# Performance work log

Hardware: AMD Instinct MI355X
Metric: run time of the kernel (lower is better)

## Reference

```python
import jax, jax.numpy as jnp
from jax import lax
import numpy as np

MAX_ATOMS = 50
MAX_DEGREE = 4
MAX_RINGS = 16
BATCH = 16384
EDGE_KEEP_PROB = 0.3  # fraction of neighbor slots that are real edges; rest are -1 (masked)


def setup_inputs() -> dict:
    key = jax.random.key(0)
    k1, k2 = jax.random.split(key)
    e = jax.random.randint(k1, (BATCH, MAX_ATOMS, MAX_DEGREE), 0, MAX_ATOMS, dtype=jnp.int32)
    keep = jax.random.uniform(k2, (BATCH, MAX_ATOMS, MAX_DEGREE)) < EDGE_KEEP_PROB
    edge = jnp.where(keep, e, jnp.int32(-1))
    return {"edge": edge}


def reference(edge):
    B, A, D = edge.shape
    N = A + 1  # node 0 is the masked-edge sentinel after +1 shift and zero-row pad
    bidx = jnp.arange(B)
    # masked_edges: shift indices by +1, pad a zero row at atom index 0 -> [B, N, D]
    me = jnp.pad(edge.astype(jnp.int32) + 1, ((0, 0), (1, 0), (0, 0)))

    # per-node state, shape [B, N]
    lnf = jnp.ones((B, N), jnp.int32).at[:, 0].set(0).at[:, 1].set(0)  # leaf_not_found
    nnv = jnp.ones((B, N), jnp.int32).at[:, 0].set(0)                  # node_not_visited
    Tree = jnp.zeros((B, N), jnp.int32)                                 # parent pointers
    num_rings = jnp.zeros((B,), jnp.int32)
    ring_idx = jnp.zeros((B, N, 2), jnp.int32)

    def visit(state, visiting):
        lnf, nnv, Tree, num_rings, ring_idx = state
        for d in range(D):  # small static degree loop (4)
            nxt = me[bidx, visiting, d]                 # [B]
            slnf = lnf[bidx, nxt]                       # specific_leaf_not_found
            slnv = nnv[bidx, nxt]                       # specific_leaf_not_visited
            cyc = (1 - slnf) * slnv * (nxt != 0).astype(jnp.int32)  # cycle_found
            ring_idx = ring_idx.at[bidx, num_rings, 0].add(visiting * cyc)
            ring_idx = ring_idx.at[bidx, num_rings, 1].add(nxt * cyc)
            num_rings = num_rings + cyc
            Tree = Tree.at[bidx, nxt].add(slnf * visiting)
            lnf = lnf.at[bidx, nxt].set(0)
        nnv = nnv.at[bidx, visiting].set(0)
        return (lnf, nnv, Tree, num_rings, ring_idx)

    # atom_idx == 1: visit node 1 (special-cased init above)
    state = visit((lnf, nnv, Tree, num_rings, ring_idx), jnp.ones((B,), jnp.int32))

    def atom_body(_, state):
        lnf, nnv = state[0], state[1]
        visiting = jnp.argmax(nnv * (1 - lnf), axis=-1).astype(jnp.int32)
        return visit(state, visiting)

    state = lax.fori_loop(2, A + 1, atom_body, state)
    lnf, nnv, Tree, num_rings, ring_idx = state

    max_num_rings = jnp.max(num_rings)
    rings = jnp.zeros((B, MAX_RINGS, A), jnp.int32)

    def ring_body(carry):
        i, rings = carry
        air = jnp.zeros((B,), jnp.int32)  # atom_in_ring_idx

        # branch 0: mark ancestor chain of ring endpoint 0
        start = ring_idx[:, i, 0]
        vb0 = jnp.zeros((B, N), jnp.int32).at[bidx, start].set(1)
        def mark0(_, c):
            vb0, start = c
            nxt = Tree[bidx, start]
            return (vb0.at[bidx, nxt].set(1), nxt)
        vb0, _ = lax.fori_loop(0, A, mark0, (vb0, start))

        # branch 1: walk ancestor chain of endpoint 1, emit atoms until chains meet
        start = ring_idx[:, i, 1]
        vb1 = jnp.zeros((B, N), jnp.int32).at[bidx, start].set(1)
        rings = rings.at[bidx, i, air].set(start)
        def b1(_, c):
            rings, vb1, start, air = c
            nxt = Tree[bidx, start]
            same = jnp.any(vb0 * vb1 == 1, axis=-1)
            nsv = (~same).astype(jnp.int32)
            air = air + nsv
            rings = rings.at[bidx, i, air].add(nxt * nsv)
            vb1 = vb1.at[bidx, nxt].set(1)
            return (rings, vb1, nxt, air)
        rings, vb1, _, air = lax.fori_loop(0, A, b1, (rings, vb1, start, air))

        # branch 2: walk endpoint-0 chain again, emit atoms until it meets branch 1
        start = ring_idx[:, i, 0]
        vb0b = jnp.zeros((B, N), jnp.int32).at[bidx, start].set(1)
        air = air + 1
        rings = rings.at[bidx, i, air].set(start)
        def b2(_, c):
            rings, vb0b, start, air = c
            nxt = Tree[bidx, start]
            vb0b = vb0b.at[bidx, nxt].set(1)
            same = jnp.any(vb0b * vb1 == 1, axis=-1)
            nsv = (~same).astype(jnp.int32)
            air = air + nsv
            rings = rings.at[bidx, i, air].add(nxt * nsv)
            return (rings, vb0b, nxt, air)
        rings, _, _, _ = lax.fori_loop(0, A, b2, (rings, vb0b, start, air))
        return (i + 1, rings)

    def ring_cond(carry):
        return carry[0] < max_num_rings

    _, rings = lax.while_loop(ring_cond, ring_body, (jnp.int32(0), rings))
    return (Tree, ring_idx, rings - 1)
```

## Files before the change

kernel.cpp:

```cpp
#include <hip/hip_runtime.h>
#include <stdint.h>

constexpr int BATCH = 16384;
constexpr int A     = 50;
constexpr int NN    = 51;
constexpr int MAXR  = 16;
constexpr int EPW   = 8;
constexpr int WPB   = 4;

__device__ __forceinline__ void prep_row(int lane, int dep,
    int s0lo, int s0hi, int s1lo, int s1hi, int pack, int i,
    int& pos, int& ta, int& tua, int& s0v)
{
    const uint64_t s0 = ((uint64_t)(uint32_t)__builtin_amdgcn_readlane(s0hi, i) << 32)
                      |  (uint32_t)__builtin_amdgcn_readlane(s0lo, i);
    const uint64_t s1 = ((uint64_t)(uint32_t)__builtin_amdgcn_readlane(s1hi, i) << 32)
                      |  (uint32_t)__builtin_amdgcn_readlane(s1lo, i);
    const int pk = __builtin_amdgcn_readlane(pack, i);
    const int dm = pk & 0xff, ds0 = (pk >> 8) & 0xff, ds1 = (pk >> 16) & 0xff;
    s0v = (pk >> 24) & 0xff;
    ta  = ds1 - dm;
    tua = ta + ds0 - dm;
    const bool on1 = ((s1 >> lane) & 1) && (dep >= dm);
    const bool on0 = ((s0 >> lane) & 1) && (dep >  dm);
    int p = on1 ? (ds1 - dep) : on0 ? (ta + 1 + ds0 - dep) : 63;
    pos = p < 63 ? p : 63;
}

__global__ __launch_bounds__(WPB * 64)
void fused_kernel(const int* __restrict__ edge, int* __restrict__ out)
{
    const int lane  = threadIdx.x & 63;
    const int wid   = threadIdx.x >> 6;
    const int gbase = (blockIdx.x * WPB + wid) * EPW;

    __shared__ uint32_t eds [WPB][EPW][NN];
    __shared__ uint16_t comb[WPB][EPW][128];

    {
        const uint4 z = make_uint4(0, 0, 0, 0);
        uint4* c16 = (uint4*)&comb[wid][0][0];
        c16[lane]      = z;
        c16[lane + 64] = z;
    }
    {
        const int4* e4 = (const int4*)edge + (size_t)gbase * A;
        #pragma unroll
        for (int k = 0; k < 7; ++k) {
            const int gi = k * 64 + lane;
            if (gi < EPW * A) {
                const int4 v = e4[gi];
                const int el = gi / A, n = gi - A * el;
                eds[wid][el][n] = (uint32_t)(v.x + 1) | ((uint32_t)(v.y + 1) << 8)
                                | ((uint32_t)(v.z + 1) << 16) | ((uint32_t)(v.w + 1) << 24);
            }
        }
    }

    const int  e  = lane >> 3;
    const int  d8 = lane & 7;
    const int  d  = d8 & 3;
    const bool hi = d8 >= 4;

    uint64_t L = (((uint64_t)1 << NN) - 1) & ~(uint64_t)3;
    uint64_t V = (((uint64_t)1 << NN) - 1) & ~(uint64_t)1;
    uint64_t M = 2;
    int visiting = 1, nr = 0;
    uint32_t w = eds[wid][e][0];

    #pragma unroll 1
    for (int it = 0; it < A; ++it) {
        const int n0 = w & 0xff, n1 = (w >> 8) & 0xff, n2 = (w >> 16) & 0xff, n3 = w >> 24;
        const uint64_t bu = ((uint64_t)1 << n0) | ((uint64_t)1 << n1)
                          | ((uint64_t)1 << n2) | ((uint64_t)1 << n3);
        const int myn = (w >> (8 * d)) & 0xff;
        const uint64_t bm = (uint64_t)1 << myn;
        const uint64_t visbit = (uint64_t)1 << visiting;
        const uint64_t Mn = (M | (V & bu)) & ~visbit;
        const bool dn = (Mn == 0);
        const uint64_t Msafe = dn ? (uint64_t)2 : Mn;
        const int nv = (int)__builtin_ctzll(Msafe);
        const uint32_t wn = eds[wid][e][nv - 1];
        const bool dup = ((d > 0) & (myn == n0)) | ((d > 1) & (myn == n1)) | ((d > 2) & (myn == n2));
        const bool fa  = ((L & bm) == 0) | dup;
        const bool cf  = fa & ((V & bm) != 0) & (myn != 0);
        const bool cb  = cf & !hi;
        const uint64_t Bc = __ballot(cb);
        const uint32_t qb = (uint32_t)(Bc >> (lane & 56)) & 0xfu;
        const int slot = nr + __builtin_popcount(qb & ((1u << d) - 1));
        nr += __builtin_popcount(qb);
        const bool p  = hi ? (cf & (slot < NN)) : !fa;
        const int idx = hi ? (64 + slot) : myn;
        if (p) comb[wid][e][idx] = (uint16_t)(visiting | (hi ? (myn << 8) : 0));
        L &= ~bu;
        V &= ~visbit;
        M = Mn; visiting = nv;
        w = dn ? 0u : wn;
        if (__ballot(!dn) == 0) break;
    }

    int*  otree = out;
    int2* oridx = (int2*)(out + (size_t)BATCH * NN);

    uint64_t MkE[EPW];
    int gE[EPW], r01E[EPW];
    #pragma unroll
    for (int e2 = 0; e2 < EPW; ++e2) {
        const int b = gbase + e2;
        const int f = (lane < NN) ? (int)comb[wid][e2][lane] : 0;
        const uint32_t pv = (lane < NN) ? (uint32_t)comb[wid][e2][64 + lane] : 0;
        MkE[e2] = ((uint64_t)1 << lane) | ((uint64_t)1 << f);
        gE[e2]  = f;
        r01E[e2] = (int)pv;
        if (lane < NN) {
            otree[(size_t)b * NN + lane] = f;
            oridx[(size_t)b * NN + lane] = make_int2((int)(pv & 0xff), (int)(pv >> 8));
        }
    }
    #pragma unroll
    for (int j6 = 0; j6 < 6; ++j6) {
        int lo8[EPW], hi8[EPW], gg8[EPW];
        #pragma unroll
        for (int e2 = 0; e2 < EPW; ++e2) {
            const int ad = gE[e2] << 2;
            lo8[e2] = __builtin_amdgcn_ds_bpermute(ad, (int)(uint32_t)MkE[e2]);
            hi8[e2] = __builtin_amdgcn_ds_bpermute(ad, (int)(MkE[e2] >> 32));
            gg8[e2] = (j6 < 5) ? __builtin_amdgcn_ds_bpermute(ad, gE[e2]) : gE[e2];
        }
        #pragma unroll
        for (int e2 = 0; e2 < EPW; ++e2) {
            MkE[e2] |= ((uint64_t)(uint32_t)hi8[e2] << 32) | (uint32_t)lo8[e2];
            gE[e2]   = gg8[e2];
        }
    }
    int depE[EPW], nactE[EPW], packE[EPW];
    int s0loE[EPW], s0hiE[EPW], s1loE[EPW], s1hiE[EPW];
    {
        int t0l[EPW], t0h[EPW], t1l[EPW], t1h[EPW];
        #pragma unroll
        for (int e2 = 0; e2 < EPW; ++e2) {
            const int Mlo = (int)(uint32_t)MkE[e2], Mhi = (int)(MkE[e2] >> 32);
            const int a0 = (r01E[e2] & 0xff) << 2, a1 = ((r01E[e2] >> 8) & 0xff) << 2;
            t0l[e2] = __builtin_amdgcn_ds_bpermute(a0, Mlo);
            t0h[e2] = __builtin_amdgcn_ds_bpermute(a0, Mhi);
            t1l[e2] = __builtin_amdgcn_ds_bpermute(a1, Mlo);
            t1h[e2] = __builtin_amdgcn_ds_bpermute(a1, Mhi);
        }
        #pragma unroll
        for (int e2 = 0; e2 < EPW; ++e2) {
            const uint64_t set0 = ((uint64_t)(uint32_t)t0h[e2] << 32) | (uint32_t)t0l[e2];
            const uint64_t set1 = ((uint64_t)(uint32_t)t1h[e2] << 32) | (uint32_t)t1l[e2];
            depE[e2] = __builtin_popcountll(MkE[e2]) - 1;
            const int dm  = __builtin_popcountll(set0 & set1) - 1;
            const int ds0 = __builtin_popcountll(set0) - 1;
            const int ds1 = __builtin_popcountll(set1) - 1;
            const int r0  = r01E[e2] & 0xff;
            s0loE[e2] = (int)(uint32_t)set0;  s0hiE[e2] = (int)(set0 >> 32);
            s1loE[e2] = (int)(uint32_t)set1;  s1hiE[e2] = (int)(set1 >> 32);
            packE[e2] = dm | (ds0 << 8) | (ds1 << 16) | (r0 << 24);
            nactE[e2] = __popcll(__ballot((lane < MAXR) && (r0 != 0)));
        }
    }

    #pragma unroll
    for (int j = 0; j < EPW; ++j) {
        const int b = gbase + j;
        int* orings = out + (size_t)BATCH * NN * 3 + (size_t)b * (MAXR * A);
        const int nact = nactE[j];
        const int dep  = depE[j];

        int i = 0;
        for (; i + 3 < nact; i += 4) {
            int p0,t0,u0,v0, p1,t1,u1,v1, p2,t2,u2,v2, p3,t3,u3,v3;
            prep_row(lane, dep, s0loE[j], s0hiE[j], s1loE[j], s1hiE[j], packE[j], i+0, p0,t0,u0,v0);
            prep_row(lane, dep, s0loE[j], s0hiE[j], s1loE[j], s1hiE[j], packE[j], i+1, p1,t1,u1,v1);
            prep_row(lane, dep, s0loE[j], s0hiE[j], s1loE[j], s1hiE[j], packE[j], i+2, p2,t2,u2,v2);
            prep_row(lane, dep, s0loE[j], s0hiE[j], s1loE[j], s1hiE[j], packE[j], i+3, p3,t3,u3,v3);
            const int m0 = __builtin_amdgcn_ds_permute(p0 << 2, lane);
            const int m1 = __builtin_amdgcn_ds_permute(p1 << 2, lane);
            const int m2 = __builtin_amdgcn_ds_permute(p2 << 2, lane);
            const int m3 = __builtin_amdgcn_ds_permute(p3 << 2, lane);
            const int r0v = (lane == t0 + 1) ? v0 : (lane <= u0 ? m0 : 0);
            const int r1v = (lane == t1 + 1) ? v1 : (lane <= u1 ? m1 : 0);
            const int r2v = (lane == t2 + 1) ? v2 : (lane <= u2 ? m2 : 0);
            const int r3v = (lane == t3 + 1) ? v3 : (lane <= u3 ? m3 : 0);
            if (lane < A) {
                orings[(i + 0) * A + lane] = r0v - 1;
                orings[(i + 1) * A + lane] = r1v - 1;
                orings[(i + 2) * A + lane] = r2v - 1;
                orings[(i + 3) * A + lane] = r3v - 1;
            }
        }
        for (; i < nact; ++i) {
            int p0, t0, u0, v0;
            prep_row(lane, dep, s0loE[j], s0hiE[j], s1loE[j], s1hiE[j], packE[j], i, p0,t0,u0,v0);
            const int m0 = __builtin_amdgcn_ds_permute(p0 << 2, lane);
            const int r0v = (lane == t0 + 1) ? v0 : (lane <= u0 ? m0 : 0);
            if (lane < A) orings[i * A + lane] = r0v - 1;
        }
        const int startw = nact * A;
        int2* p2w = (int2*)(orings + startw);
        const int n2 = (MAXR * A - startw) >> 1;
        for (int k = lane; k < n2; k += 64) p2w[k] = make_int2(-1, -1);
    }
}

extern "C" void kernel_launch(void* const* d_in, const int* in_sizes, int n_in,
                              void* d_out, int out_size, void* d_ws, size_t ws_size,
                              hipStream_t stream) {
    const int* edge = (const int*)d_in[0];
    int* out = (int*)d_out;
    hipLaunchKernelGGL(fused_kernel, dim3(BATCH / (EPW * WPB)), dim3(WPB * 64), 0, stream,
                       edge, out);
}
```

Before: 30.37 us.

## Share serial DFS across block, compact lane mapping, split post-processing per wave

Restructures work distribution: each block now handles 16 molecules, and a single wave runs the serial DFS for all 16 at once with 4 lanes per molecule instead of 8. The other waves sit idle at a barrier during that phase. Afterwards all four waves split the tree-depth and ring-emission phase, 4 molecules each, halving per-wave register arrays and adding an occupancy hint to launch bounds. The aim is to cut duplicated high-lane work in the DFS and the register pressure of the post phase, at the cost of block barriers and three idle waves during the DFS.

```diff
diff --git a/kernel.cpp b/kernel.cpp
--- a/kernel.cpp
+++ b/kernel.cpp
@@ -5,7 +5,8 @@
 constexpr int A     = 50;
 constexpr int NN    = 51;
 constexpr int MAXR  = 16;
-constexpr int EPW   = 8;
+constexpr int EPB   = 16;
+constexpr int EPWB  = 4;
 constexpr int WPB   = 4;
 
 __device__ __forceinline__ void prep_row(int lane, int dep,
@@ -27,91 +28,94 @@
     pos = p < 63 ? p : 63;
 }
 
-__global__ __launch_bounds__(WPB * 64)
+__global__ __launch_bounds__(WPB * 64, 4)
 void fused_kernel(const int* __restrict__ edge, int* __restrict__ out)
 {
-    const int lane  = threadIdx.x & 63;
-    const int wid   = threadIdx.x >> 6;
-    const int gbase = (blockIdx.x * WPB + wid) * EPW;
-
-    __shared__ uint32_t eds [WPB][EPW][NN];
-    __shared__ uint16_t comb[WPB][EPW][128];
+    const int tid   = threadIdx.x;
+    const int bbase = blockIdx.x * EPB;
+
+    __shared__ uint32_t eds [EPB][NN];
+    __shared__ uint16_t comb[EPB][128];
 
     {
-        const uint4 z = make_uint4(0, 0, 0, 0);
-        uint4* c16 = (uint4*)&comb[wid][0][0];
-        c16[lane]      = z;
-        c16[lane + 64] = z;
+        ((uint4*)&comb[0][0])[tid] = make_uint4(0, 0, 0, 0);
     }
     {
-        const int4* e4 = (const int4*)edge + (size_t)gbase * A;
-        #pragma unroll
-        for (int k = 0; k < 7; ++k) {
-            const int gi = k * 64 + lane;
-            if (gi < EPW * A) {
+        const int4* e4 = (const int4*)edge + (size_t)bbase * A;
+        #pragma unroll
+        for (int k = 0; k < 4; ++k) {
+            const int gi = k * 256 + tid;
+            if (gi < EPB * A) {
                 const int4 v = e4[gi];
                 const int el = gi / A, n = gi - A * el;
-                eds[wid][el][n] = (uint32_t)(v.x + 1) | ((uint32_t)(v.y + 1) << 8)
-                                | ((uint32_t)(v.z + 1) << 16) | ((uint32_t)(v.w + 1) << 24);
+                eds[el][n] = (uint32_t)(v.x + 1) | ((uint32_t)(v.y + 1) << 8)
+                           | ((uint32_t)(v.z + 1) << 16) | ((uint32_t)(v.w + 1) << 24);
             }
         }
     }
-
-    const int  e  = lane >> 3;
-    const int  d8 = lane & 7;
-    const int  d  = d8 & 3;
-    const bool hi = d8 >= 4;
-
-    uint64_t L = (((uint64_t)1 << NN) - 1) & ~(uint64_t)3;
-    uint64_t V = (((uint64_t)1 << NN) - 1) & ~(uint64_t)1;
-    uint64_t M = 2;
-    int visiting = 1, nr = 0;
-    uint32_t w = eds[wid][e][0];
-
-    #pragma unroll 1
-    for (int it = 0; it < A; ++it) {
-        const int n0 = w & 0xff, n1 = (w >> 8) & 0xff, n2 = (w >> 16) & 0xff, n3 = w >> 24;
-        const uint64_t bu = ((uint64_t)1 << n0) | ((uint64_t)1 << n1)
-                          | ((uint64_t)1 << n2) | ((uint64_t)1 << n3);
-        const int myn = (w >> (8 * d)) & 0xff;
-        const uint64_t bm = (uint64_t)1 << myn;
-        const uint64_t visbit = (uint64_t)1 << visiting;
-        const uint64_t Mn = (M | (V & bu)) & ~visbit;
-        const bool dn = (Mn == 0);
-        const uint64_t Msafe = dn ? (uint64_t)2 : Mn;
-        const int nv = (int)__builtin_ctzll(Msafe);
-        const uint32_t wn = eds[wid][e][nv - 1];
-        const bool dup = ((d > 0) & (myn == n0)) | ((d > 1) & (myn == n1)) | ((d > 2) & (myn == n2));
-        const bool fa  = ((L & bm) == 0) | dup;
-        const bool cf  = fa & ((V & bm) != 0) & (myn != 0);
-        const bool cb  = cf & !hi;
-        const uint64_t Bc = __ballot(cb);
-        const uint32_t qb = (uint32_t)(Bc >> (lane & 56)) & 0xfu;
-        const int slot = nr + __builtin_popcount(qb & ((1u << d) - 1));
-        nr += __builtin_popcount(qb);
-        const bool p  = hi ? (cf & (slot < NN)) : !fa;
-        const int idx = hi ? (64 + slot) : myn;
-        if (p) comb[wid][e][idx] = (uint16_t)(visiting | (hi ? (myn << 8) : 0));
-        L &= ~bu;
-        V &= ~visbit;
-        M = Mn; visiting = nv;
-        w = dn ? 0u : wn;
-        if (__ballot(!dn) == 0) break;
-    }
+    __syncthreads();
+
+    if (tid < 64) {
+        const int e = tid >> 2;
+        const int d = tid & 3;
+
+        uint64_t L = (((uint64_t)1 << NN) - 1) & ~(uint64_t)3;
+        uint64_t V = (((uint64_t)1 << NN) - 1) & ~(uint64_t)1;
+        uint64_t M = 2;
+        int visiting = 1, nr = 0;
+        uint32_t w = eds[e][0];
+
+        #pragma unroll 1
+        for (int it = 0; it < A; ++it) {
+            const int n0 = w & 0xff, n1 = (w >> 8) & 0xff, n2 = (w >> 16) & 0xff, n3 = w >> 24;
+            const uint64_t bu = ((uint64_t)1 << n0) | ((uint64_t)1 << n1)
+                              | ((uint64_t)1 << n2) | ((uint64_t)1 << n3);
+            const int myn = (w >> (8 * d)) & 0xff;
+            const uint64_t bm = (uint64_t)1 << myn;
+            const uint64_t visbit = (uint64_t)1 << visiting;
+            const uint64_t Mn = (M | (V & bu)) & ~visbit;
+            const bool dn = (Mn == 0);
+            const uint64_t Msafe = dn ? (uint64_t)2 : Mn;
+            const int nv = (int)__builtin_ctzll(Msafe);
+            const uint32_t wn = eds[e][nv - 1];
+            const bool dup = ((d > 0) & (myn == n0)) | ((d > 1) & (myn == n1)) | ((d > 2) & (myn == n2));
+            const bool fa  = ((L & bm) == 0) | dup;
+            const bool cf  = fa & ((V & bm) != 0) & (myn != 0);
+            const uint64_t Bc = __ballot(cf);
+            const uint32_t qb = (uint32_t)(Bc >> (tid & 60)) & 0xfu;
+            const int slot = nr + __builtin_popcount(qb & ((1u << d) - 1));
+            nr += __builtin_popcount(qb);
+            if (!fa) comb[e][myn] = (uint16_t)visiting;
+            if (cf && slot < NN)
+                comb[e][64 + slot] = (uint16_t)(visiting | (myn << 8));
+            L &= ~bu;
+            V &= ~visbit;
+            M = Mn; visiting = nv;
+            w = dn ? 0u : wn;
+            if (__ballot(!dn) == 0) break;
+        }
+    }
+    __syncthreads();
+
+    const int lane  = tid & 63;
+    const int wid   = tid >> 6;
+    const int ebase = wid * EPWB;
+    const int gbase = bbase + ebase;
 
     int*  otree = out;
     int2* oridx = (int2*)(out + (size_t)BATCH * NN);
 
-    uint64_t MkE[EPW];
-    int gE[EPW], r01E[EPW];
+    uint64_t MkE[EPWB];
+    int gE[EPWB], r01E[EPWB];
     #pragma unroll
-    for (int e2 = 0; e2 < EPW; ++e2) {
-        const int b = gbase + e2;
-        const int f = (lane < NN) ? (int)comb[wid][e2][lane] : 0;
-        const uint32_t pv = (lane < NN) ? (uint32_t)comb[wid][e2][64 + lane] : 0;
-        MkE[e2] = ((uint64_t)1 << lane) | ((uint64_t)1 << f);
-        gE[e2]  = f;
-        r01E[e2] = (int)pv;
+    for (int j = 0; j < EPWB; ++j) {
+        const int ew = ebase + j;
+        const int b  = gbase + j;
+        const int f = (lane < NN) ? (int)comb[ew][lane] : 0;
+        const uint32_t pv = (lane < NN) ? (uint32_t)comb[ew][64 + lane] : 0;
+        MkE[j] = ((uint64_t)1 << lane) | ((uint64_t)1 << f);
+        gE[j]  = f;
+        r01E[j] = (int)pv;
         if (lane < NN) {
             otree[(size_t)b * NN + lane] = f;
             oridx[(size_t)b * NN + lane] = make_int2((int)(pv & 0xff), (int)(pv >> 8));
@@ -119,51 +123,51 @@
     }
     #pragma unroll
     for (int j6 = 0; j6 < 6; ++j6) {
-        int lo8[EPW], hi8[EPW], gg8[EPW];
-        #pragma unroll
-        for (int e2 = 0; e2 < EPW; ++e2) {
-            const int ad = gE[e2] << 2;
-            lo8[e2] = __builtin_amdgcn_ds_bpermute(ad, (int)(uint32_t)MkE[e2]);
-            hi8[e2] = __builtin_amdgcn_ds_bpermute(ad, (int)(MkE[e2] >> 32));
-            gg8[e2] = (j6 < 5) ? __builtin_amdgcn_ds_bpermute(ad, gE[e2]) : gE[e2];
-        }
-        #pragma unroll
-        for (int e2 = 0; e2 < EPW; ++e2) {
-            MkE[e2] |= ((uint64_t)(uint32_t)hi8[e2] << 32) | (uint32_t)lo8[e2];
-            gE[e2]   = gg8[e2];
-        }
-    }
-    int depE[EPW], nactE[EPW], packE[EPW];
-    int s0loE[EPW], s0hiE[EPW], s1loE[EPW], s1hiE[EPW];
+        int lo4[EPWB], hi4[EPWB], gg4[EPWB];
+        #pragma unroll
+        for (int j = 0; j < EPWB; ++j) {
+            const int ad = gE[j] << 2;
+            lo4[j] = __builtin_amdgcn_ds_bpermute(ad, (int)(uint32_t)MkE[j]);
+            hi4[j] = __builtin_amdgcn_ds_bpermute(ad, (int)(MkE[j] >> 32));
+            gg4[j] = (j6 < 5) ? __builtin_amdgcn_ds_bpermute(ad, gE[j]) : gE[j];
+        }
+        #pragma unroll
+        for (int j = 0; j < EPWB; ++j) {
+            MkE[j] |= ((uint64_t)(uint32_t)hi4[j] << 32) | (uint32_t)lo4[j];
+            gE[j]   = gg4[j];
+        }
+    }
+    int depE[EPWB], nactE[EPWB], packE[EPWB];
+    int s0loE[EPWB], s0hiE[EPWB], s1loE[EPWB], s1hiE[EPWB];
     {
-        int t0l[EPW], t0h[EPW], t1l[EPW], t1h[EPW];
-        #pragma unroll
-        for (int e2 = 0; e2 < EPW; ++e2) {
-            const int Mlo = (int)(uint32_t)MkE[e2], Mhi = (int)(MkE[e2] >> 32);
-            const int a0 = (r01E[e2] & 0xff) << 2, a1 = ((r01E[e2] >> 8) & 0xff) << 2;
-            t0l[e2] = __builtin_amdgcn_ds_bpermute(a0, Mlo);
-            t0h[e2] = __builtin_amdgcn_ds_bpermute(a0, Mhi);
-            t1l[e2] = __builtin_amdgcn_ds_bpermute(a1, Mlo);
-            t1h[e2] = __builtin_amdgcn_ds_bpermute(a1, Mhi);
-        }
-        #pragma unroll
-        for (int e2 = 0; e2 < EPW; ++e2) {
-            const uint64_t set0 = ((uint64_t)(uint32_t)t0h[e2] << 32) | (uint32_t)t0l[e2];
-            const uint64_t set1 = ((uint64_t)(uint32_t)t1h[e2] << 32) | (uint32_t)t1l[e2];
-            depE[e2] = __builtin_popcountll(MkE[e2]) - 1;
+        int t0l[EPWB], t0h[EPWB], t1l[EPWB], t1h[EPWB];
+        #pragma unroll
+        for (int j = 0; j < EPWB; ++j) {
+            const int Mlo = (int)(uint32_t)MkE[j], Mhi = (int)(MkE[j] >> 32);
+            const int a0 = (r01E[j] & 0xff) << 2, a1 = ((r01E[j] >> 8) & 0xff) << 2;
+            t0l[j] = __builtin_amdgcn_ds_bpermute(a0, Mlo);
+            t0h[j] = __builtin_amdgcn_ds_bpermute(a0, Mhi);
+            t1l[j] = __builtin_amdgcn_ds_bpermute(a1, Mlo);
+            t1h[j] = __builtin_amdgcn_ds_bpermute(a1, Mhi);
+        }
+        #pragma unroll
+        for (int j = 0; j < EPWB; ++j) {
+            const uint64_t set0 = ((uint64_t)(uint32_t)t0h[j] << 32) | (uint32_t)t0l[j];
+            const uint64_t set1 = ((uint64_t)(uint32_t)t1h[j] << 32) | (uint32_t)t1l[j];
+            depE[j] = __builtin_popcountll(MkE[j]) - 1;
             const int dm  = __builtin_popcountll(set0 & set1) - 1;
             const int ds0 = __builtin_popcountll(set0) - 1;
             const int ds1 = __builtin_popcountll(set1) - 1;
-            const int r0  = r01E[e2] & 0xff;
-            s0loE[e2] = (int)(uint32_t)set0;  s0hiE[e2] = (int)(set0 >> 32);
-            s1loE[e2] = (int)(uint32_t)set1;  s1hiE[e2] = (int)(set1 >> 32);
-            packE[e2] = dm | (ds0 << 8) | (ds1 << 16) | (r0 << 24);
-            nactE[e2] = __popcll(__ballot((lane < MAXR) && (r0 != 0)));
+            const int r0  = r01E[j] & 0xff;
+            s0loE[j] = (int)(uint32_t)set0;  s0hiE[j] = (int)(set0 >> 32);
+            s1loE[j] = (int)(uint32_t)set1;  s1hiE[j] = (int)(set1 >> 32);
+            packE[j] = dm | (ds0 << 8) | (ds1 << 16) | (r0 << 24);
+            nactE[j] = __popcll(__ballot((lane < MAXR) && (r0 != 0)));
         }
     }
 
     #pragma unroll
-    for (int j = 0; j < EPW; ++j) {
+    for (int j = 0; j < EPWB; ++j) {
         const int b = gbase + j;
         int* orings = out + (size_t)BATCH * NN * 3 + (size_t)b * (MAXR * A);
         const int nact = nactE[j];
@@ -210,6 +214,6 @@
                               hipStream_t stream) {
     const int* edge = (const int*)d_in[0];
     int* out = (int*)d_out;
-    hipLaunchKernelGGL(fused_kernel, dim3(BATCH / (EPW * WPB)), dim3(WPB * 64), 0, stream,
+    hipLaunchKernelGGL(fused_kernel, dim3(BATCH / EPB), dim3(WPB * 64), 0, stream,
                        edge, out);
 }
```

Result: faster. 26.88 us (-11.5%).
